# Performance work log

Hardware: AMD Instinct MI355X
Metric: run time of the kernel (lower is better)

The kernel has to match this reference:

```python
import jax, jax.numpy as jnp
import numpy as np

NEG_SLOPE = 0.2
N_NODES = 50000


def _gat_layer(x, src, dst, invalid, W, al, ar, b):
    # x: [N, Fin]; src/dst: [E] (self-loops appended); invalid: [E] bool
    N = x.shape[0]
    H, F = al.shape
    z = (x @ W).reshape(N, H, F)                       # [N,H,F]
    el = jnp.sum(z * al[None], axis=-1)                # [N,H]
    er = jnp.sum(z * ar[None], axis=-1)                # [N,H]
    e = el[src] + er[dst]                              # [E,H]
    e = jnp.where(e > 0, e, NEG_SLOPE * e)             # LeakyReLU(0.2)
    e = jnp.where(invalid[:, None], -jnp.inf, e)       # removed self-loop edges
    # edge softmax per destination node (every node has a self-loop -> max finite)
    m = jax.ops.segment_max(e, dst, num_segments=N)    # [N,H]
    ex = jnp.exp(e - m[dst])
    ex = jnp.where(invalid[:, None], 0.0, ex)
    s = jax.ops.segment_sum(ex, dst, num_segments=N)   # [N,H]
    alpha = ex / s[dst]                                # [E,H]
    msg = z[src] * alpha[:, :, None]                   # [E,H,F]
    out = jax.ops.segment_sum(msg, dst, num_segments=N)  # [N,H,F]
    out = out + b.reshape(1, H, F)
    return jax.nn.elu(out)


def _with_self_loops(src, dst):
    N = N_NODES
    loop = jnp.arange(N, dtype=src.dtype)
    invalid = jnp.concatenate([src == dst, jnp.zeros(N, dtype=bool)])
    return jnp.concatenate([src, loop]), jnp.concatenate([dst, loop]), invalid


def setup_inputs() -> dict:
    key = jax.random.key(0)
    ks = jax.random.split(key, 12)
    N, Fin, H0, F0, H1, C = N_NODES, 256, 4, 32, 1, 40
    E = 800000
    sc = lambda k, shp, fan: jax.random.normal(k, shp, jnp.float32) * (1.0 / np.sqrt(fan))
    return {
        "x": jax.random.normal(ks[0], (N, Fin), jnp.float32),
        "src": jax.random.randint(ks[1], (E,), 0, N, jnp.int32),
        "dst": jax.random.randint(ks[2], (E,), 0, N, jnp.int32),
        "W0": sc(ks[3], (Fin, H0 * F0), Fin),
        "al0": sc(ks[4], (H0, F0), F0),
        "ar0": sc(ks[5], (H0, F0), F0),
        "b0": jnp.zeros((H0 * F0,), jnp.float32),
        "W1": sc(ks[6], (H0 * F0, H1 * C), H0 * F0),
        "al1": sc(ks[7], (H1, C), C),
        "ar1": sc(ks[8], (H1, C), C),
        "b1": jnp.zeros((C,), jnp.float32),
    }


def reference(x, src, dst, W0, al0, ar0, b0, W1, al1, ar1, b1):
    s, d, invalid = _with_self_loops(src, dst)
    h = _gat_layer(x, s, d, invalid, W0, al0, ar0, b0)   # [N,4,32]
    h = h.reshape(h.shape[0], -1)                        # flatten(1) -> [N,128]
    h = _gat_layer(h, s, d, invalid, W1, al1, ar1, b1)   # [N,1,40]
    return h.mean(axis=1)                                # mean over heads -> [N,40]
```

## Files before the change

kernel.cpp:

```cpp
#include <hip/hip_runtime.h>
#include <stdint.h>

#define NN 50000
#define EE 800000
#define CAP 48
#define NXCD 8
#define NPX 6250
#define EPB 4096
#define NCHUNK 196
#define GB0 782

typedef __bf16 bf16x8 __attribute__((ext_vector_type(8)));
typedef float  f32x4  __attribute__((ext_vector_type(4)));

__device__ __forceinline__ float bflo(unsigned int w){ union{unsigned int i;float f;}c; c.i=w<<16; return c.f; }
__device__ __forceinline__ float bfhi(unsigned int w){ union{unsigned int i;float f;}c; c.i=w&0xFFFF0000u; return c.f; }
__device__ __forceinline__ bf16x8 bf8_zero(){
  bf16x8 v;
  #pragma unroll
  for (int j=0;j<8;++j) v[j]=(__bf16)0.f;
  return v;
}

__global__ __launch_bounds__(256) void k_prep(const float* __restrict__ W0,
                                              __bf16* __restrict__ Wg,
                                              int* __restrict__ cursor,
                                              int* __restrict__ csrv){
  int tg = blockIdx.x*256 + threadIdx.x;
  if (tg < 4096){
    int k8 = tg >> 7, n = tg & 127;
    bf16x8 v;
    #pragma unroll
    for (int j=0;j<8;++j) v[j] = (__bf16)W0[(k8*8+j)*128 + n];
    *(bf16x8*)(Wg + ((size_t)(k8*128 + n))*8) = v;
  }
  if (tg < NN){
    cursor[tg] = 1;
    csrv[(size_t)tg*CAP] = tg;
  }
}

__global__ __launch_bounds__(256) void k_gemm0_scatter(const float* __restrict__ x,
    const __bf16* __restrict__ Wg, const float* __restrict__ al0, const float* __restrict__ ar0,
    __bf16* __restrict__ z0b, float* __restrict__ el0, float* __restrict__ er0,
    const int* __restrict__ src, const int* __restrict__ dst,
    int* __restrict__ cursor, int* __restrict__ csrv){
  if (blockIdx.x >= GB0){
    const int xcd = blockIdx.x & 7;
    const int chunk = (blockIdx.x - GB0) >> 3;
    const int lo = xcd*NPX, hi = lo + NPX;
    int e0 = chunk*EPB + threadIdx.x*4;
    #pragma unroll
    for (int it=0; it<EPB/1024; ++it, e0 += 1024){
      if (e0 < EE){
        int4 d4 = *(const int4*)(dst + e0);
        int dv[4] = {d4.x, d4.y, d4.z, d4.w};
        #pragma unroll
        for (int j=0;j<4;++j){
          int d = dv[j];
          if (d >= lo && d < hi){
            int s = src[e0 + j];
            unsigned int inv = (s==d) ? 0x80000000u : 0u;
            int pos = atomicAdd(&cursor[d], 1);
            csrv[(size_t)d*CAP + pos] = (int)((unsigned int)s | inv);
          }
        }
      }
    }
    return;
  }
  const int tid = threadIdx.x;
  const int wv = tid >> 6, ln = tid & 63, q = ln >> 4, mr = ln & 15;
  const int nhalf = wv & 1, mhalf = wv >> 1;
  const int m0w = blockIdx.x*64 + mhalf*32;
  const int n0w = nhalf*64;
  f32x4 acc[2][4];
  #pragma unroll
  for (int mt=0;mt<2;++mt)
    #pragma unroll
    for (int nt=0;nt<4;++nt) acc[mt][nt] = (f32x4){0.f,0.f,0.f,0.f};
  const bool av0 = (m0w + mr) < NN;
  const bool av1 = (m0w + 16 + mr) < NN;
  const float* xr0 = x + (size_t)(m0w + mr)*256;
  const float* xr1 = x + (size_t)(m0w + 16 + mr)*256;
  #pragma unroll
  for (int kc=0;kc<8;++kc){
    int ko = kc*32 + q*8;
    bf16x8 a0 = bf8_zero(), a1 = bf8_zero();
    if (av0){
      float4 p = *(const float4*)(xr0 + ko);
      float4 p2 = *(const float4*)(xr0 + ko + 4);
      a0[0]=(__bf16)p.x; a0[1]=(__bf16)p.y; a0[2]=(__bf16)p.z; a0[3]=(__bf16)p.w;
      a0[4]=(__bf16)p2.x; a0[5]=(__bf16)p2.y; a0[6]=(__bf16)p2.z; a0[7]=(__bf16)p2.w;
    }
    if (av1){
      float4 p = *(const float4*)(xr1 + ko);
      float4 p2 = *(const float4*)(xr1 + ko + 4);
      a1[0]=(__bf16)p.x; a1[1]=(__bf16)p.y; a1[2]=(__bf16)p.z; a1[3]=(__bf16)p.w;
      a1[4]=(__bf16)p2.x; a1[5]=(__bf16)p2.y; a1[6]=(__bf16)p2.z; a1[7]=(__bf16)p2.w;
    }
    const __bf16* wb = Wg + ((size_t)((kc*4+q)*128 + n0w + mr))*8;
    #pragma unroll
    for (int nt=0;nt<4;++nt){
      bf16x8 bf = *(const bf16x8*)(wb + (size_t)nt*16*8);
      acc[0][nt] = __builtin_amdgcn_mfma_f32_16x16x32_bf16(a0, bf, acc[0][nt], 0,0,0);
      acc[1][nt] = __builtin_amdgcn_mfma_f32_16x16x32_bf16(a1, bf, acc[1][nt], 0,0,0);
    }
  }
  float alv[4], arv[4];
  #pragma unroll
  for (int nt=0;nt<4;++nt){ int c = n0w + nt*16 + mr; alv[nt]=al0[c]; arv[nt]=ar0[c]; }
  #pragma unroll
  for (int mt=0;mt<2;++mt){
    #pragma unroll
    for (int r=0;r<4;++r){
      int grow = m0w + mt*16 + q*4 + r;
      if (grow < NN){
        #pragma unroll
        for (int nt=0;nt<4;++nt)
          z0b[(size_t)grow*128 + n0w + nt*16 + mr] = (__bf16)acc[mt][nt][r];
      }
      float pl0 = acc[mt][0][r]*alv[0] + acc[mt][1][r]*alv[1];
      float pr0 = acc[mt][0][r]*arv[0] + acc[mt][1][r]*arv[1];
      float pl1 = acc[mt][2][r]*alv[2] + acc[mt][3][r]*alv[3];
      float pr1 = acc[mt][2][r]*arv[2] + acc[mt][3][r]*arv[3];
      #pragma unroll
      for (int off=1; off<16; off<<=1){
        pl0 += __shfl_xor(pl0, off, 16); pr0 += __shfl_xor(pr0, off, 16);
        pl1 += __shfl_xor(pl1, off, 16); pr1 += __shfl_xor(pr1, off, 16);
      }
      if (mr==0 && grow<NN){
        el0[grow*4 + 2*nhalf]   = pl0; er0[grow*4 + 2*nhalf]   = pr0;
        el0[grow*4 + 2*nhalf+1] = pl1; er0[grow*4 + 2*nhalf+1] = pr1;
      }
    }
  }
}

__global__ __launch_bounds__(256) void k_agg0(const unsigned short* __restrict__ z0b,
    const float* __restrict__ el0, const float* __restrict__ er0,
    const int* __restrict__ cursor, const int* __restrict__ csrv,
    const float* __restrict__ b0, unsigned short* __restrict__ hb){
  int lane = threadIdx.x & 63;
  int i = __builtin_amdgcn_readfirstlane(blockIdx.x*4 + (threadIdx.x >> 6));
  int h1 = lane >> 4;
  int lane2 = lane << 1;
  const float erv = er0[(size_t)i*4 + h1];
  float ax=0.f, ay=0.f, s=0.f;
  int p = i*CAP, pe = p + cursor[i];
  for (; p+8<=pe; p+=8){
    int4 va = *(const int4*)(csrv + p);
    int4 vb = *(const int4*)(csrv + p + 4);
    int v[8] = {va.x,va.y,va.z,va.w,vb.x,vb.y,vb.z,vb.w};
    float el[8];
    #pragma unroll
    for (int j=0;j<8;++j) el[j] = el0[(size_t)(v[j]&0x7FFFFFFF)*4 + h1];
    unsigned int zw[8];
    #pragma unroll
    for (int j=0;j<8;++j)
      zw[j] = *(const unsigned int*)(z0b + (size_t)(v[j]&0x7FFFFFFF)*128 + lane2);
    #pragma unroll
    for (int j=0;j<8;++j){
      float e = el[j] + erv;
      e = fmaxf(e, 0.2f*e);
      float w = (v[j] < 0) ? 0.f : __expf(e);
      s += w; ax = fmaf(w, bflo(zw[j]), ax); ay = fmaf(w, bfhi(zw[j]), ay);
    }
  }
  for (; p+4<=pe; p+=4){
    int4 va = *(const int4*)(csrv + p);
    int v[4] = {va.x,va.y,va.z,va.w};
    float el[4];
    #pragma unroll
    for (int j=0;j<4;++j) el[j] = el0[(size_t)(v[j]&0x7FFFFFFF)*4 + h1];
    unsigned int zw[4];
    #pragma unroll
    for (int j=0;j<4;++j)
      zw[j] = *(const unsigned int*)(z0b + (size_t)(v[j]&0x7FFFFFFF)*128 + lane2);
    #pragma unroll
    for (int j=0;j<4;++j){
      float e = el[j] + erv;
      e = fmaxf(e, 0.2f*e);
      float w = (v[j] < 0) ? 0.f : __expf(e);
      s += w; ax = fmaf(w, bflo(zw[j]), ax); ay = fmaf(w, bfhi(zw[j]), ay);
    }
  }
  for (; p<pe; ++p){
    int v = csrv[p];
    int u = v & 0x7FFFFFFF;
    float e = el0[(size_t)u*4 + h1] + erv;
    e = fmaxf(e, 0.2f*e);
    float w = (v < 0) ? 0.f : __expf(e);
    unsigned int zw = *(const unsigned int*)(z0b + (size_t)u*128 + lane2);
    s += w; ax = fmaf(w, bflo(zw), ax); ay = fmaf(w, bfhi(zw), ay);
  }
  float inv = 1.f/s;
  float ox = ax*inv + b0[lane*2], oy = ay*inv + b0[lane*2+1];
  ox = ox>0.f?ox:__expf(ox)-1.f; oy = oy>0.f?oy:__expf(oy)-1.f;
  union { __bf16 b[2]; unsigned int u; } pk;
  pk.b[0]=(__bf16)ox; pk.b[1]=(__bf16)oy;
  *(unsigned int*)(hb + (size_t)i*128 + lane2) = pk.u;
}

__global__ __launch_bounds__(256) void k_gemm1(const __bf16* __restrict__ hb,
    const float* __restrict__ W1, const float* __restrict__ al1, const float* __restrict__ ar1,
    __bf16* __restrict__ z1b, float* __restrict__ el1, float* __restrict__ er1){
  __shared__ __bf16 Blds[16][48][8];
  const int tid = threadIdx.x;
  for (int t=tid; t<16*48*8; t+=256) (&Blds[0][0][0])[t] = (__bf16)0.f;
  __syncthreads();
  for (int t=tid; t<5120; t+=256){
    int k = t/40, n = t - k*40;
    Blds[k>>3][n][k&7] = (__bf16)W1[t];
  }
  __syncthreads();
  const int wm = tid >> 6, ln = tid & 63, q = ln >> 4, mr = ln & 15;
  const int m0 = blockIdx.x*64 + wm*16;
  const int arow = m0 + mr;
  const bool av = (arow < NN);
  f32x4 acc[3];
  #pragma unroll
  for (int nt=0;nt<3;++nt) acc[nt] = (f32x4){0.f,0.f,0.f,0.f};
  #pragma unroll
  for (int kc=0;kc<4;++kc){
    bf16x8 af = bf8_zero();
    if (av) af = *(const bf16x8*)(hb + (size_t)arow*128 + kc*32 + q*8);
    #pragma unroll
    for (int nt=0;nt<3;++nt){
      bf16x8 bf = *(const bf16x8*)&Blds[kc*4+q][nt*16+mr][0];
      acc[nt] = __builtin_amdgcn_mfma_f32_16x16x32_bf16(af, bf, acc[nt], 0,0,0);
    }
  }
  float alv[3], arv[3];
  #pragma unroll
  for (int nt=0;nt<3;++nt){
    int c = nt*16+mr;
    alv[nt] = (c<40) ? al1[c] : 0.f;
    arv[nt] = (c<40) ? ar1[c] : 0.f;
  }
  #pragma unroll
  for (int r=0;r<4;++r){
    int grow = m0 + q*4 + r;
    if (grow < NN){
      #pragma unroll
      for (int nt=0;nt<3;++nt){
        int c = nt*16+mr;
        if (c < 40) z1b[(size_t)grow*40 + c] = (__bf16)acc[nt][r];
      }
    }
    float pl = acc[0][r]*alv[0] + acc[1][r]*alv[1] + acc[2][r]*alv[2];
    float pr = acc[0][r]*arv[0] + acc[1][r]*arv[1] + acc[2][r]*arv[2];
    #pragma unroll
    for (int off=1; off<16; off<<=1){ pl += __shfl_xor(pl, off, 16); pr += __shfl_xor(pr, off, 16); }
    if (mr==0 && grow<NN){ el1[grow]=pl; er1[grow]=pr; }
  }
}

__global__ __launch_bounds__(256) void k_agg1(const unsigned short* __restrict__ z1b,
    const float* __restrict__ el1, const float* __restrict__ er1,
    const int* __restrict__ cursor, const int* __restrict__ csrv,
    const float* __restrict__ b1, float* __restrict__ out){
  int lane = threadIdx.x & 63;
  int i = __builtin_amdgcn_readfirstlane(blockIdx.x*4 + (threadIdx.x >> 6));
  int fl = (lane < 20) ? (lane<<1) : 0;
  const float erv = er1[i];
  float ax=0.f, ay=0.f, s=0.f;
  int p = i*CAP, pe = p + cursor[i];
  for (; p+8<=pe; p+=8){
    int4 va = *(const int4*)(csrv + p);
    int4 vb = *(const int4*)(csrv + p + 4);
    int v[8] = {va.x,va.y,va.z,va.w,vb.x,vb.y,vb.z,vb.w};
    float el[8];
    #pragma unroll
    for (int j=0;j<8;++j) el[j] = el1[v[j]&0x7FFFFFFF];
    unsigned int zw[8];
    #pragma unroll
    for (int j=0;j<8;++j)
      zw[j] = *(const unsigned int*)(z1b + (size_t)(v[j]&0x7FFFFFFF)*40 + fl);
    #pragma unroll
    for (int j=0;j<8;++j){
      float e = el[j] + erv;
      e = fmaxf(e, 0.2f*e);
      float w = (v[j] < 0) ? 0.f : __expf(e);
      s += w; ax = fmaf(w, bflo(zw[j]), ax); ay = fmaf(w, bfhi(zw[j]), ay);
    }
  }
  for (; p+4<=pe; p+=4){
    int4 va = *(const int4*)(csrv + p);
    int v[4] = {va.x,va.y,va.z,va.w};
    float el[4];
    #pragma unroll
    for (int j=0;j<4;++j) el[j] = el1[v[j]&0x7FFFFFFF];
    unsigned int zw[4];
    #pragma unroll
    for (int j=0;j<4;++j)
      zw[j] = *(const unsigned int*)(z1b + (size_t)(v[j]&0x7FFFFFFF)*40 + fl);
    #pragma unroll
    for (int j=0;j<4;++j){
      float e = el[j] + erv;
      e = fmaxf(e, 0.2f*e);
      float w = (v[j] < 0) ? 0.f : __expf(e);
      s += w; ax = fmaf(w, bflo(zw[j]), ax); ay = fmaf(w, bfhi(zw[j]), ay);
    }
  }
  for (; p<pe; ++p){
    int v = csrv[p];
    int u = v & 0x7FFFFFFF;
    float e = el1[u] + erv;
    e = fmaxf(e, 0.2f*e);
    float w = (v < 0) ? 0.f : __expf(e);
    unsigned int zw = *(const unsigned int*)(z1b + (size_t)u*40 + fl);
    s += w; ax = fmaf(w, bflo(zw), ax); ay = fmaf(w, bfhi(zw), ay);
  }
  if (lane < 20){
    float inv = 1.f/s;
    float ox = ax*inv + b1[lane*2], oy = ay*inv + b1[lane*2+1];
    ox = ox>0.f?ox:__expf(ox)-1.f; oy = oy>0.f?oy:__expf(oy)-1.f;
    *(float2*)(out + (size_t)i*40 + (lane<<1)) = make_float2(ox, oy);
  }
}

extern "C" void kernel_launch(void* const* d_in, const int* in_sizes, int n_in,
                              void* d_out, int out_size, void* d_ws, size_t ws_size,
                              hipStream_t stream){
  const float* x   = (const float*)d_in[0];
  const int*   src = (const int*)d_in[1];
  const int*   dst = (const int*)d_in[2];
  const float* W0  = (const float*)d_in[3];
  const float* al0 = (const float*)d_in[4];
  const float* ar0 = (const float*)d_in[5];
  const float* b0  = (const float*)d_in[6];
  const float* W1  = (const float*)d_in[7];
  const float* al1 = (const float*)d_in[8];
  const float* ar1 = (const float*)d_in[9];
  const float* b1  = (const float*)d_in[10];
  float* out = (float*)d_out;

  __bf16* z0b = (__bf16*)d_ws;
  __bf16* hb  = z0b + (size_t)NN*128;
  __bf16* z1b = hb  + (size_t)NN*128;
  __bf16* Wg  = z1b + (size_t)NN*40;
  float* el0 = (float*)(Wg + 32768);
  float* er0 = el0 + (size_t)NN*4;
  float* el1 = er0 + (size_t)NN*4;
  float* er1 = el1 + NN;
  int* cursor = (int*)(er1 + NN);
  int* csrv   = cursor + NN;

  k_prep<<<(NN+255)/256, 256, 0, stream>>>(W0, Wg, cursor, csrv);
  k_gemm0_scatter<<<GB0 + NCHUNK*NXCD, 256, 0, stream>>>(x, Wg, al0, ar0, z0b, el0, er0,
                                                         src, dst, cursor, csrv);
  k_agg0 <<<NN/4, 256, 0, stream>>>((const unsigned short*)z0b, el0, er0, cursor, csrv, b0, (unsigned short*)hb);
  k_gemm1<<<(NN+63)/64, 256, 0, stream>>>(hb, W1, al1, ar1, z1b, el1, er1);
  k_agg1 <<<NN/4, 256, 0, stream>>>((const unsigned short*)z1b, el1, er1, cursor, csrv, b1, out);
}
```

Measured before the change: 224.6 us.

## Fuse layer-1 projection GEMM into layer-0 aggregation kernel via LDS tile

Layer-0 aggregation now writes each block's four output rows into shared memory. One wavefront then runs the layer-1 MFMA projection on them, writing z1, el1 and er1 directly. This removes the hb intermediate round trip through global memory and one kernel launch. W1 is pre-packed to bf16 in the prep kernel, and the 16-row MFMA tile uses only 4 real rows, so most of the MFMA work is wasted and a block barrier is added to the aggregation.

```diff
diff --git a/kernel.cpp b/kernel.cpp
--- a/kernel.cpp
+++ b/kernel.cpp
@@ -23,7 +23,9 @@
 }
 
 __global__ __launch_bounds__(256) void k_prep(const float* __restrict__ W0,
+                                              const float* __restrict__ W1,
                                               __bf16* __restrict__ Wg,
+                                              __bf16* __restrict__ Wg1,
                                               int* __restrict__ cursor,
                                               int* __restrict__ csrv){
   int tg = blockIdx.x*256 + threadIdx.x;
@@ -33,6 +35,13 @@
     #pragma unroll
     for (int j=0;j<8;++j) v[j] = (__bf16)W0[(k8*8+j)*128 + n];
     *(bf16x8*)(Wg + ((size_t)(k8*128 + n))*8) = v;
+  } else if (tg < 4096 + 768){
+    int idx = tg - 4096;
+    int k16 = idx / 48, n = idx - k16*48;
+    bf16x8 v;
+    #pragma unroll
+    for (int j=0;j<8;++j) v[j] = (n < 40) ? (__bf16)W1[(k16*8+j)*40 + n] : (__bf16)0.f;
+    *(bf16x8*)(Wg1 + (size_t)idx*8) = v;
   }
   if (tg < NN){
     cursor[tg] = 1;
@@ -137,12 +146,21 @@
   }
 }
 
-__global__ __launch_bounds__(256) void k_agg0(const unsigned short* __restrict__ z0b,
+__global__ __launch_bounds__(256) void k_agg0g1(const unsigned short* __restrict__ z0b,
     const float* __restrict__ el0, const float* __restrict__ er0,
     const int* __restrict__ cursor, const int* __restrict__ csrv,
-    const float* __restrict__ b0, unsigned short* __restrict__ hb){
+    const float* __restrict__ b0, const __bf16* __restrict__ Wg1,
+    const float* __restrict__ al1, const float* __restrict__ ar1,
+    __bf16* __restrict__ z1b, float* __restrict__ el1, float* __restrict__ er1){
+  __shared__ __bf16 hsh[16][136];
+  unsigned int* hshu = (unsigned int*)&hsh[0][0];
+  #pragma unroll
+  for (int t = threadIdx.x; t < 12*68; t += 256) hshu[4*68 + t] = 0u;
+
   int lane = threadIdx.x & 63;
-  int i = __builtin_amdgcn_readfirstlane(blockIdx.x*4 + (threadIdx.x >> 6));
+  int wv = threadIdx.x >> 6;
+  int i0 = __builtin_amdgcn_readfirstlane(blockIdx.x*4);
+  int i = i0 + wv;
   int h1 = lane >> 4;
   int lane2 = lane << 1;
   const float erv = er0[(size_t)i*4 + h1];
@@ -199,60 +217,46 @@
   ox = ox>0.f?ox:__expf(ox)-1.f; oy = oy>0.f?oy:__expf(oy)-1.f;
   union { __bf16 b[2]; unsigned int u; } pk;
   pk.b[0]=(__bf16)ox; pk.b[1]=(__bf16)oy;
-  *(unsigned int*)(hb + (size_t)i*128 + lane2) = pk.u;
-}
-
-__global__ __launch_bounds__(256) void k_gemm1(const __bf16* __restrict__ hb,
-    const float* __restrict__ W1, const float* __restrict__ al1, const float* __restrict__ ar1,
-    __bf16* __restrict__ z1b, float* __restrict__ el1, float* __restrict__ er1){
-  __shared__ __bf16 Blds[16][48][8];
-  const int tid = threadIdx.x;
-  for (int t=tid; t<16*48*8; t+=256) (&Blds[0][0][0])[t] = (__bf16)0.f;
+  hshu[wv*68 + lane] = pk.u;
   __syncthreads();
-  for (int t=tid; t<5120; t+=256){
-    int k = t/40, n = t - k*40;
-    Blds[k>>3][n][k&7] = (__bf16)W1[t];
-  }
-  __syncthreads();
-  const int wm = tid >> 6, ln = tid & 63, q = ln >> 4, mr = ln & 15;
-  const int m0 = blockIdx.x*64 + wm*16;
-  const int arow = m0 + mr;
-  const bool av = (arow < NN);
-  f32x4 acc[3];
-  #pragma unroll
-  for (int nt=0;nt<3;++nt) acc[nt] = (f32x4){0.f,0.f,0.f,0.f};
-  #pragma unroll
-  for (int kc=0;kc<4;++kc){
-    bf16x8 af = bf8_zero();
-    if (av) af = *(const bf16x8*)(hb + (size_t)arow*128 + kc*32 + q*8);
-    #pragma unroll
-    for (int nt=0;nt<3;++nt){
-      bf16x8 bf = *(const bf16x8*)&Blds[kc*4+q][nt*16+mr][0];
-      acc[nt] = __builtin_amdgcn_mfma_f32_16x16x32_bf16(af, bf, acc[nt], 0,0,0);
-    }
-  }
-  float alv[3], arv[3];
-  #pragma unroll
-  for (int nt=0;nt<3;++nt){
-    int c = nt*16+mr;
-    alv[nt] = (c<40) ? al1[c] : 0.f;
-    arv[nt] = (c<40) ? ar1[c] : 0.f;
-  }
-  #pragma unroll
-  for (int r=0;r<4;++r){
-    int grow = m0 + q*4 + r;
-    if (grow < NN){
+
+  if (wv == 0){
+    const int q = lane >> 4, mr = lane & 15;
+    f32x4 acc1[3];
+    #pragma unroll
+    for (int nt=0;nt<3;++nt) acc1[nt] = (f32x4){0.f,0.f,0.f,0.f};
+    #pragma unroll
+    for (int kc=0;kc<4;++kc){
+      bf16x8 af = *(const bf16x8*)&hsh[mr][kc*32 + q*8];
       #pragma unroll
       for (int nt=0;nt<3;++nt){
-        int c = nt*16+mr;
-        if (c < 40) z1b[(size_t)grow*40 + c] = (__bf16)acc[nt][r];
-      }
-    }
-    float pl = acc[0][r]*alv[0] + acc[1][r]*alv[1] + acc[2][r]*alv[2];
-    float pr = acc[0][r]*arv[0] + acc[1][r]*arv[1] + acc[2][r]*arv[2];
-    #pragma unroll
-    for (int off=1; off<16; off<<=1){ pl += __shfl_xor(pl, off, 16); pr += __shfl_xor(pr, off, 16); }
-    if (mr==0 && grow<NN){ el1[grow]=pl; er1[grow]=pr; }
+        bf16x8 bf = *(const bf16x8*)(Wg1 + ((size_t)((kc*4+q)*48 + nt*16+mr))*8);
+        acc1[nt] = __builtin_amdgcn_mfma_f32_16x16x32_bf16(af, bf, acc1[nt], 0,0,0);
+      }
+    }
+    float alv[3], arv[3];
+    #pragma unroll
+    for (int nt=0;nt<3;++nt){
+      int c = nt*16+mr;
+      alv[nt] = (c<40) ? al1[c] : 0.f;
+      arv[nt] = (c<40) ? ar1[c] : 0.f;
+    }
+    #pragma unroll
+    for (int r=0;r<4;++r){
+      if (q == 0){
+        int grow = i0 + r;
+        #pragma unroll
+        for (int nt=0;nt<3;++nt){
+          int c = nt*16+mr;
+          if (c < 40) z1b[(size_t)grow*40 + c] = (__bf16)acc1[nt][r];
+        }
+      }
+      float pl = acc1[0][r]*alv[0] + acc1[1][r]*alv[1] + acc1[2][r]*alv[2];
+      float pr = acc1[0][r]*arv[0] + acc1[1][r]*arv[1] + acc1[2][r]*arv[2];
+      #pragma unroll
+      for (int off=1; off<16; off<<=1){ pl += __shfl_xor(pl, off, 16); pr += __shfl_xor(pr, off, 16); }
+      if (q==0 && mr==0){ el1[i0+r]=pl; er1[i0+r]=pr; }
+    }
   }
 }
 
@@ -337,20 +341,20 @@
   float* out = (float*)d_out;
 
   __bf16* z0b = (__bf16*)d_ws;
-  __bf16* hb  = z0b + (size_t)NN*128;
-  __bf16* z1b = hb  + (size_t)NN*128;
+  __bf16* z1b = z0b + (size_t)NN*128;
   __bf16* Wg  = z1b + (size_t)NN*40;
-  float* el0 = (float*)(Wg + 32768);
+  __bf16* Wg1 = Wg + 32768;
+  float* el0 = (float*)(Wg1 + 6144);
   float* er0 = el0 + (size_t)NN*4;
   float* el1 = er0 + (size_t)NN*4;
   float* er1 = el1 + NN;
   int* cursor = (int*)(er1 + NN);
   int* csrv   = cursor + NN;
 
-  k_prep<<<(NN+255)/256, 256, 0, stream>>>(W0, Wg, cursor, csrv);
+  k_prep<<<(NN+255)/256, 256, 0, stream>>>(W0, W1, Wg, Wg1, cursor, csrv);
   k_gemm0_scatter<<<GB0 + NCHUNK*NXCD, 256, 0, stream>>>(x, Wg, al0, ar0, z0b, el0, er0,
                                                          src, dst, cursor, csrv);
-  k_agg0 <<<NN/4, 256, 0, stream>>>((const unsigned short*)z0b, el0, er0, cursor, csrv, b0, (unsigned short*)hb);
-  k_gemm1<<<(NN+63)/64, 256, 0, stream>>>(hb, W1, al1, ar1, z1b, el1, er1);
+  k_agg0g1<<<NN/4, 256, 0, stream>>>((const unsigned short*)z0b, el0, er0, cursor, csrv, b0,
+                                     Wg1, al1, ar1, z1b, el1, er1);
   k_agg1 <<<NN/4, 256, 0, stream>>>((const unsigned short*)z1b, el1, er1, cursor, csrv, b1, out);
 }
```

Result: slower. 238.7 us (+6.3%).
